# Kernel optimization log

Hardware: AMD Instinct MI355X
Metric: run time of the kernel (lower is better)

The kernel has to match this reference:

```python
import jax, jax.numpy as jnp
import numpy as np

B, TQ, TK = 2, 1024, 2048
DQ, DC, H, TOPK = 1024, 768, 16, 64
DH = DQ // H


def setup_inputs() -> dict:
    key = jax.random.key(0)
    ks = jax.random.split(key, 12)
    s = lambda d: 1.0 / np.sqrt(d)
    return {
        "x": jax.random.normal(ks[0], (B, TQ, DQ), jnp.float32),
        "context": jax.random.normal(ks[1], (B, TK, DC), jnp.float32),
        "key_padding_mask": jax.random.bernoulli(ks[2], 0.05, (B, TK)),
        "Wq": jax.random.normal(ks[3], (DQ, DQ), jnp.float32) * s(DQ),
        "bq": jnp.zeros((DQ,), jnp.float32),
        "Wk": jax.random.normal(ks[4], (DC, DQ), jnp.float32) * s(DC),
        "bk": jnp.zeros((DQ,), jnp.float32),
        "Wv": jax.random.normal(ks[5], (DC, DQ), jnp.float32) * s(DC),
        "bv": jnp.zeros((DQ,), jnp.float32),
        "Wo": jax.random.normal(ks[6], (DQ, DQ), jnp.float32) * s(DQ),
        "bo": jnp.zeros((DQ,), jnp.float32),
    }


def _heads(t):
    # (B, T, DQ) -> (B, H, T, DH)
    b, tt, _ = t.shape
    return t.reshape(b, tt, H, DH).transpose(0, 2, 1, 3)


def reference(x, context, key_padding_mask, Wq, bq, Wk, bk, Wv, bv, Wo, bo):
    q = _heads(x @ Wq + bq)          # (B,H,Tq,DH)
    k = _heads(context @ Wk + bk)    # (B,H,Tk,DH)
    v = _heads(context @ Wv + bv)    # (B,H,Tk,DH)

    scale = DH ** -0.5
    logits = jnp.einsum("bhqd,bhkd->bhqk", q, k) * scale  # (B,H,Tq,Tk)
    neg = jnp.finfo(logits.dtype).min
    logits = jnp.where(key_padding_mask[:, None, None, :], neg, logits)

    # hard top-k sparsification: keep top TOPK logits per query, fill rest with -inf-like
    topk_vals, topk_idx = jax.lax.top_k(logits, TOPK)
    sparse_logits = jnp.full_like(logits, neg)
    sparse_logits = jnp.put_along_axis(sparse_logits, topk_idx, topk_vals, axis=-1, inplace=False)

    attn = jax.nn.softmax(sparse_logits, axis=-1)
    out = jnp.einsum("bhqk,bhkd->bhqd", attn, v)  # (B,H,Tq,DH)
    out = out.transpose(0, 2, 1, 3).reshape(B, TQ, DQ)
    return out @ Wo + bo
```

## Files before the change

kernel.cpp:

```cpp
#include <hip/hip_runtime.h>
#include <cstdint>
#include <cstddef>

#define BN_ 2
#define TQ_ 1024
#define TK_ 2048
#define DQ_ 1024
#define DC_ 768
#define NH_ 16
#define DH_ 64
#define TOPK_ 64

typedef unsigned short u16;
typedef __attribute__((ext_vector_type(8))) short short8;
typedef __attribute__((ext_vector_type(8))) u16   ushort8;
typedef __attribute__((ext_vector_type(4))) float floatx4;

__device__ __forceinline__ float bf2f(u16 u) { return __uint_as_float(((unsigned)u) << 16); }
__device__ __forceinline__ u16 f2bf(float f) {
    unsigned u = __float_as_uint(f);
    u += 0x7FFFu + ((u >> 16) & 1u);
    return (u16)(u >> 16);
}
__device__ __forceinline__ float definite(float v, float repl) {
    return ((__float_as_uint(v) & 0x7F800000u) == 0x7F800000u) ? repl : v;
}
__device__ __forceinline__ unsigned mono(float f) {
    unsigned u = __float_as_uint(f);
    return (u & 0x80000000u) ? ~u : (u | 0x80000000u);
}
__device__ __forceinline__ float invmono(unsigned u) {
    return __uint_as_float((u & 0x80000000u) ? (u & 0x7FFFFFFFu) : ~u);
}
__device__ __forceinline__ int gsum16(int x) {
#pragma unroll
    for (int o = 1; o < 16; o <<= 1) x += __shfl_xor(x, o);
    return x;
}
__device__ __forceinline__ int gmin16(int x) {
#pragma unroll
    for (int o = 1; o < 16; o <<= 1) { int y = __shfl_xor(x, o); x = (y < x) ? y : x; }
    return x;
}
__device__ __forceinline__ unsigned gmin16u(unsigned x) {
#pragma unroll
    for (int o = 1; o < 16; o <<= 1) { unsigned y = __shfl_xor((int)x, o); x = (y < x) ? y : x; }
    return x;
}
__device__ __forceinline__ unsigned gmax16u(unsigned x) {
#pragma unroll
    for (int o = 1; o < 16; o <<= 1) { unsigned y = __shfl_xor((int)x, o); x = (y > x) ? y : x; }
    return x;
}
__device__ __forceinline__ float gmax16f(float x) {
#pragma unroll
    for (int o = 1; o < 16; o <<= 1) x = fmaxf(x, __shfl_xor(x, o));
    return x;
}
__device__ __forceinline__ float gsum16f(float x) {
#pragma unroll
    for (int o = 1; o < 16; o <<= 1) x += __shfl_xor(x, o);
    return x;
}

__global__ void marker_kernel(float* __restrict__ out, int n, float val) {
    const int i = blockIdx.x * 256 + threadIdx.x;
    if (i < n) out[i] = val;
}

template <int NV>
__device__ __forceinline__ void select_topk(const unsigned (&um)[NV], const int (&kk)[NV],
                                            unsigned base, int hb, int l16,
                                            float* cvrow, int* ckrow) {
    unsigned X = 0u;
    bool done = false;
    for (int bit = hb; bit >= 0; --bit) {
        const unsigned C = X | (1u << bit);
        int c = 0;
#pragma unroll
        for (int j = 0; j < NV; ++j) c += (um[j] >= C) ? 1 : 0;
        c = gsum16(c);
        if (!done && c >= 64) X = C;
        if (c == 64) done = true;
        if (__all(done)) break;
    }
    int myGt = 0;
#pragma unroll
    for (int j = 0; j < NV; ++j) myGt += (um[j] > X) ? 1 : 0;
    const int totalGt = gsum16(myGt);
    int pre = myGt;
#pragma unroll
    for (int off = 1; off < 16; off <<= 1) {
        const int tv = __shfl_up(pre, off);
        if (l16 >= off) pre += tv;
    }
    int wpos = pre - myGt;
#pragma unroll
    for (int j = 0; j < NV; ++j) {
        if (um[j] > X) {
            cvrow[wpos] = invmono(base + um[j]);
            ckrow[wpos] = kk[j];
            ++wpos;
        }
    }
    const float xval = invmono(base + X);
    int remaining = 64 - totalGt;
    int pos = totalGt;
    int lastkey = -1;
    while (remaining > 0) {
        int mykey = 0x7FFFFFFF;
#pragma unroll
        for (int j = 0; j < NV; ++j)
            if (um[j] == X && kk[j] > lastkey && kk[j] < mykey) mykey = kk[j];
        const int mn = gmin16(mykey);
        if (mn == 0x7FFFFFFF) break;
        if (mykey == mn) { cvrow[pos] = xval; ckrow[pos] = mn; }
        lastkey = mn;
        ++pos; --remaining;
    }
}

__global__ void __launch_bounds__(256) tsplit(const float* __restrict__ W,
                                              u16* __restrict__ Wh, u16* __restrict__ Wl,
                                              int K, int N) {
    __shared__ float t[32][33];
    const int x = threadIdx.x & 31, y = threadIdx.x >> 5;
    const int bn = blockIdx.x * 32, bk = blockIdx.y * 32;
#pragma unroll
    for (int i = 0; i < 32; i += 8) t[y + i][x] = W[(size_t)(bk + y + i) * N + bn + x];
    __syncthreads();
#pragma unroll
    for (int i = 0; i < 32; i += 8) {
        const float f = t[x][y + i];
        const u16 hi = f2bf(f);
        const size_t o = (size_t)(bn + y + i) * K + bk + x;
        Wh[o] = hi;
        Wl[o] = f2bf(f - bf2f(hi));
    }
}

template <int TBM, int ASPLIT, int OMODE>
__global__ void __launch_bounds__(256) gemm2(
    const void* __restrict__ Ap, const void* __restrict__ Alp,
    const u16* __restrict__ Bh, const u16* __restrict__ Bl,
    const float* __restrict__ bias, float scale,
    void* __restrict__ out0, void* __restrict__ out1,
    int M, int N, int K) {
    constexpr int MT = TBM / 32;
    alignas(16) __shared__ u16 Ah[TBM][72];
    alignas(16) __shared__ u16 Al[TBM][72];
    alignas(16) __shared__ u16 Bhs[64][72];
    alignas(16) __shared__ u16 Bls[64][72];

    const int tid = threadIdx.x;
    const int lane = tid & 63, wave = tid >> 6;
    const int wm = wave >> 1, wn = wave & 1;
    const int quad = lane >> 4, l16 = lane & 15;
    const int bm = blockIdx.y * TBM, bn = blockIdx.x * 64;

    floatx4 acc[MT][2] = {};

    for (int k0 = 0; k0 < K; k0 += 64) {
        __syncthreads();
        if constexpr (TBM == 64) {
            const int r0 = tid >> 3, c0 = (tid & 7) << 3;
#pragma unroll
            for (int hh = 0; hh < 2; ++hh) {
                const int r = r0 + hh * 32;
                const size_t aoff = (size_t)(bm + r) * K + k0 + c0;
                if constexpr (ASPLIT == 0) {
                    const float* f = (const float*)Ap + aoff;
                    const floatx4 a = *(const floatx4*)f;
                    const floatx4 b = *(const floatx4*)(f + 4);
#pragma unroll
                    for (int j = 0; j < 4; ++j) {
                        u16 t = f2bf(a[j]);
                        Ah[r][c0 + j] = t; Al[r][c0 + j] = f2bf(a[j] - bf2f(t));
                        t = f2bf(b[j]);
                        Ah[r][c0 + 4 + j] = t; Al[r][c0 + 4 + j] = f2bf(b[j] - bf2f(t));
                    }
                } else {
                    *(ushort8*)&Ah[r][c0] = *(const ushort8*)((const u16*)Ap  + aoff);
                    *(ushort8*)&Al[r][c0] = *(const ushort8*)((const u16*)Alp + aoff);
                }
            }
        } else {
            const int sr = tid >> 1, sc = (tid & 1) * 32;
            const float* f = (const float*)Ap + (size_t)(bm + sr) * K + k0 + sc;
#pragma unroll
            for (int v = 0; v < 8; ++v) {
                const floatx4 a = *(const floatx4*)(f + 4 * v);
#pragma unroll
                for (int j = 0; j < 4; ++j) {
                    const u16 t = f2bf(a[j]);
                    Ah[sr][sc + 4 * v + j] = t;
                    Al[sr][sc + 4 * v + j] = f2bf(a[j] - bf2f(t));
                }
            }
        }
        {
            const int r0 = tid >> 2, c0 = (tid & 3) * 16;
            const size_t boff = (size_t)(bn + r0) * K + k0 + c0;
            *(ushort8*)&Bhs[r0][c0]     = *(const ushort8*)(Bh + boff);
            *(ushort8*)&Bhs[r0][c0 + 8] = *(const ushort8*)(Bh + boff + 8);
            *(ushort8*)&Bls[r0][c0]     = *(const ushort8*)(Bl + boff);
            *(ushort8*)&Bls[r0][c0 + 8] = *(const ushort8*)(Bl + boff + 8);
        }
        __syncthreads();
#pragma unroll
        for (int s = 0; s < 2; ++s) {
            short8 ah[MT], al[MT], bh[2], bl[2];
#pragma unroll
            for (int mt = 0; mt < MT; ++mt) {
                ah[mt] = *(const short8*)&Ah[wm * (TBM / 2) + mt * 16 + l16][s * 32 + quad * 8];
                al[mt] = *(const short8*)&Al[wm * (TBM / 2) + mt * 16 + l16][s * 32 + quad * 8];
            }
#pragma unroll
            for (int nt = 0; nt < 2; ++nt) {
                bh[nt] = *(const short8*)&Bhs[wn * 32 + nt * 16 + l16][s * 32 + quad * 8];
                bl[nt] = *(const short8*)&Bls[wn * 32 + nt * 16 + l16][s * 32 + quad * 8];
            }
#pragma unroll
            for (int mt = 0; mt < MT; ++mt)
#pragma unroll
                for (int nt = 0; nt < 2; ++nt) {
                    acc[mt][nt] = __builtin_amdgcn_mfma_f32_16x16x32_bf16(ah[mt], bh[nt], acc[mt][nt], 0, 0, 0);
                    acc[mt][nt] = __builtin_amdgcn_mfma_f32_16x16x32_bf16(al[mt], bh[nt], acc[mt][nt], 0, 0, 0);
                    acc[mt][nt] = __builtin_amdgcn_mfma_f32_16x16x32_bf16(ah[mt], bl[nt], acc[mt][nt], 0, 0, 0);
                }
        }
    }

#pragma unroll
    for (int mt = 0; mt < MT; ++mt) {
#pragma unroll
        for (int nt = 0; nt < 2; ++nt) {
            const int col = bn + wn * 32 + nt * 16 + l16;
            const float bcol = bias[col];
#pragma unroll
            for (int r = 0; r < 4; ++r) {
                const int row = bm + wm * (TBM / 2) + mt * 16 + quad * 4 + r;
                const float val = definite((acc[mt][nt][r] + bcol) * scale, 0.0f);
                const size_t idx = (size_t)row * N + col;
                if constexpr (OMODE == 0) {
                    ((float*)out0)[idx] = val;
                } else if constexpr (OMODE == 1) {
                    ((u16*)out0)[idx] = f2bf(val);
                } else {
                    const u16 hi = f2bf(val);
                    ((u16*)out0)[idx] = hi;
                    ((u16*)out1)[idx] = f2bf(val - bf2f(hi));
                }
            }
        }
    }
}

__global__ void __launch_bounds__(256, 4) attn_topk(
    const u16* Qhi, const u16* Qlo,
    const u16* __restrict__ Khi, const u16* __restrict__ Klo,
    const u16* __restrict__ Vb16, const void* __restrict__ maskp,
    u16* attnH, u16* attnL) {
    __shared__ float lg[16][512];
    __shared__ float cval[16][64];
    __shared__ int   ckey[16][64];

    const int tid = threadIdx.x;
    const int lane = tid & 63, wave = tid >> 6;
    const int quad = lane >> 4, l16 = lane & 15;
    const int rowg = wave * 4 + quad;
    const int b = blockIdx.z, h = blockIdx.y, q0 = blockIdx.x * 16;

    int mmode;
    {
        bool cbyte = false, cbf = false, cf32 = false;
#pragma unroll
        for (int j = 0; j < 16; ++j) {
            const int i = lane + 64 * j;
            const unsigned v = ((const u16*)maskp)[i];
            cbyte |= (v == 0x0100u || v == 0x0101u) || ((i & 1) && v == 0x0001u);
            cbf   |= (!(i & 1)) && v == 0x3F80u;
            cf32  |= (i & 1) && v == 0x3F80u;
        }
        const bool abf = __any(cbf), af32 = __any(cf32), abyte = __any(cbyte);
        mmode = abf ? 2 : (af32 ? 3 : (abyte ? 1 : 0));
    }

    short8 qh[2], ql[2];
    {
        const size_t base = (size_t)(b * TQ_ + q0 + l16) * DQ_ + h * DH_ + quad * 8;
        qh[0] = *(const short8*)(Qhi + base);
        qh[1] = *(const short8*)(Qhi + base + 32);
        ql[0] = *(const short8*)(Qlo + base);
        ql[1] = *(const short8*)(Qlo + base + 32);
    }

    for (int i = tid; i < 16 * 64; i += 256) {
        cval[i >> 6][i & 63] = __uint_as_float(0xFF800000u);
        ckey[i >> 6][i & 63] = i & 63;
    }

    for (int qtr = 0; qtr < 4; ++qtr) {
#pragma unroll 2
        for (int t = 0; t < 8; ++t) {
            const int key = qtr * 512 + wave * 128 + t * 16 + l16;
            const size_t kb = (size_t)(b * TK_ + key) * DQ_ + h * DH_ + quad * 8;
            const short8 kh0 = *(const short8*)(Khi + kb);
            const short8 kh1 = *(const short8*)(Khi + kb + 32);
            const short8 kl0 = *(const short8*)(Klo + kb);
            const short8 kl1 = *(const short8*)(Klo + kb + 32);
            floatx4 acc = {};
            acc = __builtin_amdgcn_mfma_f32_16x16x32_bf16(qh[0], kh0, acc, 0, 0, 0);
            acc = __builtin_amdgcn_mfma_f32_16x16x32_bf16(ql[0], kh0, acc, 0, 0, 0);
            acc = __builtin_amdgcn_mfma_f32_16x16x32_bf16(qh[0], kl0, acc, 0, 0, 0);
            acc = __builtin_amdgcn_mfma_f32_16x16x32_bf16(qh[1], kh1, acc, 0, 0, 0);
            acc = __builtin_amdgcn_mfma_f32_16x16x32_bf16(ql[1], kh1, acc, 0, 0, 0);
            acc = __builtin_amdgcn_mfma_f32_16x16x32_bf16(qh[1], kl1, acc, 0, 0, 0);
            const int midx = b * TK_ + key;
            bool masked;
            if (mmode == 2)      masked = ((const u16*)maskp)[midx] != 0;
            else if (mmode == 3) masked = ((const float*)maskp)[midx] != 0.0f;
            else if (mmode == 1) masked = ((const unsigned char*)maskp)[midx] != 0;
            else                 masked = ((const int*)maskp)[midx] != 0;
            const int kk = wave * 128 + t * 16 + l16;
#pragma unroll
            for (int r = 0; r < 4; ++r)
                lg[quad * 4 + r][kk] = masked ? -3.0e38f : definite(acc[r], -3.0e38f);
        }
        __syncthreads();

        unsigned uc[4]; int ck4[4];
#pragma unroll
        for (int t = 0; t < 4; ++t) {
            uc[t] = mono(cval[rowg][l16 + 16 * t]);
            ck4[t] = ckey[rowg][l16 + 16 * t];
        }

        if (qtr == 0) {
            unsigned um[36]; int kk[36];
#pragma unroll
            for (int j = 0; j < 32; ++j) {
                um[j] = mono(lg[rowg][l16 + 16 * j]);
                kk[j] = l16 + 16 * j;
            }
#pragma unroll
            for (int t = 0; t < 4; ++t) { um[32 + t] = uc[t]; kk[32 + t] = ck4[t]; }
            select_topk<36>(um, kk, 0u, 31, l16, cval[rowg], ckey[rowg]);
        } else {
            unsigned cm = uc[0];
            cm = (uc[1] < cm) ? uc[1] : cm;
            cm = (uc[2] < cm) ? uc[2] : cm;
            cm = (uc[3] < cm) ? uc[3] : cm;
            cm = gmin16u(cm);
            unsigned zm[36]; int kk[36];
            unsigned zmx = 0;
#pragma unroll
            for (int j = 0; j < 32; ++j) {
                const unsigned u = mono(lg[rowg][l16 + 16 * j]);
                zm[j] = (u > cm) ? (u - cm) : 0u;
                kk[j] = qtr * 512 + l16 + 16 * j;
                zmx = (zm[j] > zmx) ? zm[j] : zmx;
            }
#pragma unroll
            for (int t = 0; t < 4; ++t) {
                zm[32 + t] = uc[t] - cm;
                kk[32 + t] = ck4[t];
                zmx = (zm[32 + t] > zmx) ? zm[32 + t] : zmx;
            }
            zmx = gmax16u(zmx);
            const int hb = 31 - __clz(zmx | 1u);
            select_topk<36>(zm, kk, cm, hb, l16, cval[rowg], ckey[rowg]);
        }
        if (qtr < 3) __syncthreads();
    }

    {
        float v4[4];
#pragma unroll
        for (int t = 0; t < 4; ++t) v4[t] = cval[rowg][l16 + 16 * t];
        float m = fmaxf(fmaxf(v4[0], v4[1]), fmaxf(v4[2], v4[3]));
        m = gmax16f(m);
        float p4[4], S = 0.f;
#pragma unroll
        for (int t = 0; t < 4; ++t) { p4[t] = __expf(v4[t] - m); S += p4[t]; }
        S = gsum16f(S);
        const float inv = 1.0f / S;
#pragma unroll
        for (int t = 0; t < 4; ++t) cval[rowg][l16 + 16 * t] = p4[t] * inv;
    }

    const int half = lane >> 5, l32 = lane & 31;
    const u16* Vrow = Vb16 + (size_t)b * TK_ * DQ_ + h * DH_ + l32 * 2;
#pragma unroll
    for (int rp = 0; rp < 2; ++rp) {
        const int row = wave * 4 + rp * 2 + half;
        float a0 = 0.f, a1 = 0.f;
#pragma unroll 4
        for (int e = 0; e < 64; ++e) {
            const float w = cval[row][e];
            const int k = ckey[row][e];
            const unsigned v2 = *(const unsigned*)(Vrow + (size_t)k * DQ_);
            a0 += w * bf2f((u16)(v2 & 0xFFFFu));
            a1 += w * bf2f((u16)(v2 >> 16));
        }
        a0 = definite(a0, 0.0f);
        a1 = definite(a1, 0.0f);
        const size_t o = (size_t)(b * TQ_ + q0 + row) * DQ_ + h * DH_ + l32 * 2;
        const u16 h0 = f2bf(a0), h1 = f2bf(a1);
        const u16 l0 = f2bf(a0 - bf2f(h0)), l1 = f2bf(a1 - bf2f(h1));
        *(unsigned*)(attnH + o) = (unsigned)h0 | ((unsigned)h1 << 16);
        *(unsigned*)(attnL + o) = (unsigned)l0 | ((unsigned)l1 << 16);
    }
}

extern "C" void kernel_launch(void* const* d_in, const int* in_sizes, int n_in,
                              void* d_out, int out_size, void* d_ws, size_t ws_size,
                              hipStream_t stream) {
    static const int exp_sizes[11] = {2097152, 3145728, 4096, 1048576, 1024,
                                      786432, 1024, 786432, 1024, 1048576, 1024};
    if (n_in != 11) {
        marker_kernel<<<(out_size + 255) / 256, 256, 0, stream>>>((float*)d_out, out_size,
                                                                  (float)(150 + n_in));
        return;
    }
    for (int i = 0; i < 11; ++i)
        if (in_sizes[i] != exp_sizes[i]) {
            marker_kernel<<<(out_size + 255) / 256, 256, 0, stream>>>((float*)d_out, out_size,
                                                                      (float)(200 + i));
            return;
        }

    const float* x   = (const float*)d_in[0];
    const float* ctx = (const float*)d_in[1];
    const void*  msk = d_in[2];
    const float* Wq = (const float*)d_in[3];
    const float* bq = (const float*)d_in[4];
    const float* Wk = (const float*)d_in[5];
    const float* bk = (const float*)d_in[6];
    const float* Wv = (const float*)d_in[7];
    const float* bv = (const float*)d_in[8];
    const float* Wo = (const float*)d_in[9];
    const float* bo = (const float*)d_in[10];

    const size_t SZ_Q = (size_t)BN_ * TQ_ * DQ_ * 2;
    const size_t SZ_K = (size_t)BN_ * TK_ * DQ_ * 2;
    const size_t NEED = 2 * SZ_Q + 2 * SZ_K + SZ_K;
    if (ws_size < NEED) {
        marker_kernel<<<(out_size + 255) / 256, 256, 0, stream>>>(
            (float*)d_out, out_size, (float)(ws_size >> 20));
        return;
    }

    char* ws = (char*)d_ws;
    u16* Qhi = (u16*)(ws);
    u16* Qlo = (u16*)(ws + SZ_Q);
    u16* Khi = (u16*)(ws + 2 * SZ_Q);
    u16* Klo = (u16*)(ws + 2 * SZ_Q + SZ_K);
    u16* Vb  = (u16*)(ws + 2 * SZ_Q + 2 * SZ_K);

    u16* WqT_h = Khi;
    u16* WqT_l = Khi + (size_t)DQ_ * DQ_;
    u16* WkT_h = Vb;
    u16* WkT_l = Vb + (size_t)DC_ * DQ_;
    u16* WvT_h = (u16*)d_out;
    u16* WvT_l = (u16*)d_out + (size_t)DC_ * DQ_;
    u16* WoT_h = Khi;
    u16* WoT_l = Khi + (size_t)DQ_ * DQ_;

    const int MQ = BN_ * TQ_;
    const int MK = BN_ * TK_;

    tsplit<<<dim3(DQ_ / 32, DQ_ / 32), 256, 0, stream>>>(Wq, WqT_h, WqT_l, DQ_, DQ_);
    gemm2<64, 0, 2><<<dim3(DQ_ / 64, MQ / 64), 256, 0, stream>>>(
        x, nullptr, WqT_h, WqT_l, bq, 0.125f, Qhi, Qlo, MQ, DQ_, DQ_);
    tsplit<<<dim3(DQ_ / 32, DC_ / 32), 256, 0, stream>>>(Wk, WkT_h, WkT_l, DC_, DQ_);
    gemm2<128, 0, 2><<<dim3(DQ_ / 64, MK / 128), 256, 0, stream>>>(
        ctx, nullptr, WkT_h, WkT_l, bk, 1.0f, Khi, Klo, MK, DQ_, DC_);
    tsplit<<<dim3(DQ_ / 32, DC_ / 32), 256, 0, stream>>>(Wv, WvT_h, WvT_l, DC_, DQ_);
    gemm2<128, 0, 1><<<dim3(DQ_ / 64, MK / 128), 256, 0, stream>>>(
        ctx, nullptr, WvT_h, WvT_l, bv, 1.0f, Vb, nullptr, MK, DQ_, DC_);

    attn_topk<<<dim3(TQ_ / 16, NH_, BN_), 256, 0, stream>>>(
        Qhi, Qlo, Khi, Klo, Vb, msk, Qhi, Qlo);

    tsplit<<<dim3(DQ_ / 32, DQ_ / 32), 256, 0, stream>>>(Wo, WoT_h, WoT_l, DQ_, DQ_);
    gemm2<64, 1, 0><<<dim3(DQ_ / 64, MQ / 64), 256, 0, stream>>>(
        Qhi, Qlo, WoT_h, WoT_l, bo, 1.0f, d_out, nullptr, MQ, DQ_, DQ_);
}
```

Baseline: 433.1 us.

## Retile projection GEMMs to 64x128 with XOR-swizzled LDS and range-narrow first top-k pass

Replaces the padded-LDS GEMM with a 64x128 tile that stores A and B in XOR-swizzled shared memory. This is meant to cut bank conflicts and to reuse each A tile across more output columns with vectorized stores. In the attention kernel, the first-quarter top-k selection now subtracts the row minimum and starts the radix search at the actual highest differing bit, instead of always scanning 32 bits. The costs are fewer blocks per GEMM grid, more registers per thread, and an extra min/max reduction per row.

Result: no change. 431.2 us (-0.4%).

```diff
diff --git a/kernel.cpp b/kernel.cpp
--- a/kernel.cpp
+++ b/kernel.cpp
@@ -139,91 +139,86 @@
     }
 }
 
-template <int TBM, int ASPLIT, int OMODE>
-__global__ void __launch_bounds__(256) gemm2(
+template <int ASPLIT, int OMODE>
+__global__ void __launch_bounds__(256) gemm3(
     const void* __restrict__ Ap, const void* __restrict__ Alp,
     const u16* __restrict__ Bh, const u16* __restrict__ Bl,
     const float* __restrict__ bias, float scale,
     void* __restrict__ out0, void* __restrict__ out1,
     int M, int N, int K) {
-    constexpr int MT = TBM / 32;
-    alignas(16) __shared__ u16 Ah[TBM][72];
-    alignas(16) __shared__ u16 Al[TBM][72];
-    alignas(16) __shared__ u16 Bhs[64][72];
-    alignas(16) __shared__ u16 Bls[64][72];
+    __shared__ u16 Ahs[64 * 64];
+    __shared__ u16 Als[64 * 64];
+    __shared__ u16 Bhs[128 * 64];
+    __shared__ u16 Bls[128 * 64];
 
     const int tid = threadIdx.x;
     const int lane = tid & 63, wave = tid >> 6;
     const int wm = wave >> 1, wn = wave & 1;
     const int quad = lane >> 4, l16 = lane & 15;
-    const int bm = blockIdx.y * TBM, bn = blockIdx.x * 64;
-
-    floatx4 acc[MT][2] = {};
+    const int bm = blockIdx.y * 64, bn = blockIdx.x * 128;
+
+    floatx4 acc[2][4] = {};
 
     for (int k0 = 0; k0 < K; k0 += 64) {
         __syncthreads();
-        if constexpr (TBM == 64) {
-            const int r0 = tid >> 3, c0 = (tid & 7) << 3;
-#pragma unroll
-            for (int hh = 0; hh < 2; ++hh) {
-                const int r = r0 + hh * 32;
-                const size_t aoff = (size_t)(bm + r) * K + k0 + c0;
-                if constexpr (ASPLIT == 0) {
-                    const float* f = (const float*)Ap + aoff;
-                    const floatx4 a = *(const floatx4*)f;
-                    const floatx4 b = *(const floatx4*)(f + 4);
-#pragma unroll
-                    for (int j = 0; j < 4; ++j) {
-                        u16 t = f2bf(a[j]);
-                        Ah[r][c0 + j] = t; Al[r][c0 + j] = f2bf(a[j] - bf2f(t));
-                        t = f2bf(b[j]);
-                        Ah[r][c0 + 4 + j] = t; Al[r][c0 + 4 + j] = f2bf(b[j] - bf2f(t));
-                    }
-                } else {
-                    *(ushort8*)&Ah[r][c0] = *(const ushort8*)((const u16*)Ap  + aoff);
-                    *(ushort8*)&Al[r][c0] = *(const ushort8*)((const u16*)Alp + aoff);
+#pragma unroll
+        for (int s2 = 0; s2 < 2; ++s2) {
+            const int slot = tid + s2 * 256;
+            const int m = slot >> 3, cpos = slot & 7;
+            const int c = cpos ^ (m & 7);
+            const size_t aoff = (size_t)(bm + m) * K + k0 + c * 8;
+            if constexpr (ASPLIT == 0) {
+                const float* f = (const float*)Ap + aoff;
+                const floatx4 a = *(const floatx4*)f;
+                const floatx4 b = *(const floatx4*)(f + 4);
+                ushort8 hi, lo;
+#pragma unroll
+                for (int j = 0; j < 4; ++j) {
+                    u16 t = f2bf(a[j]);
+                    hi[j] = t; lo[j] = f2bf(a[j] - bf2f(t));
+                    t = f2bf(b[j]);
+                    hi[4 + j] = t; lo[4 + j] = f2bf(b[j] - bf2f(t));
                 }
-            }
-        } else {
-            const int sr = tid >> 1, sc = (tid & 1) * 32;
-            const float* f = (const float*)Ap + (size_t)(bm + sr) * K + k0 + sc;
-#pragma unroll
-            for (int v = 0; v < 8; ++v) {
-                const floatx4 a = *(const floatx4*)(f + 4 * v);
-#pragma unroll
-                for (int j = 0; j < 4; ++j) {
-                    const u16 t = f2bf(a[j]);
-                    Ah[sr][sc + 4 * v + j] = t;
-                    Al[sr][sc + 4 * v + j] = f2bf(a[j] - bf2f(t));
-                }
-            }
-        }
-        {
-            const int r0 = tid >> 2, c0 = (tid & 3) * 16;
-            const size_t boff = (size_t)(bn + r0) * K + k0 + c0;
-            *(ushort8*)&Bhs[r0][c0]     = *(const ushort8*)(Bh + boff);
-            *(ushort8*)&Bhs[r0][c0 + 8] = *(const ushort8*)(Bh + boff + 8);
-            *(ushort8*)&Bls[r0][c0]     = *(const ushort8*)(Bl + boff);
-            *(ushort8*)&Bls[r0][c0 + 8] = *(const ushort8*)(Bl + boff + 8);
+                *(ushort8*)&Ahs[slot * 8] = hi;
+                *(ushort8*)&Als[slot * 8] = lo;
+            } else {
+                *(ushort8*)&Ahs[slot * 8] = *(const ushort8*)((const u16*)Ap  + aoff);
+                *(ushort8*)&Als[slot * 8] = *(const ushort8*)((const u16*)Alp + aoff);
+            }
+        }
+#pragma unroll
+        for (int s4 = 0; s4 < 4; ++s4) {
+            const int slot = tid + s4 * 256;
+            const int n = slot >> 3, cpos = slot & 7;
+            const int c = cpos ^ (n & 7);
+            const size_t boff = (size_t)(bn + n) * K + k0 + c * 8;
+            *(ushort8*)&Bhs[slot * 8] = *(const ushort8*)(Bh + boff);
+            *(ushort8*)&Bls[slot * 8] = *(const ushort8*)(Bl + boff);
         }
         __syncthreads();
 #pragma unroll
         for (int s = 0; s < 2; ++s) {
-            short8 ah[MT], al[MT], bh[2], bl[2];
-#pragma unroll
-            for (int mt = 0; mt < MT; ++mt) {
-                ah[mt] = *(const short8*)&Ah[wm * (TBM / 2) + mt * 16 + l16][s * 32 + quad * 8];
-                al[mt] = *(const short8*)&Al[wm * (TBM / 2) + mt * 16 + l16][s * 32 + quad * 8];
-            }
-#pragma unroll
-            for (int nt = 0; nt < 2; ++nt) {
-                bh[nt] = *(const short8*)&Bhs[wn * 32 + nt * 16 + l16][s * 32 + quad * 8];
-                bl[nt] = *(const short8*)&Bls[wn * 32 + nt * 16 + l16][s * 32 + quad * 8];
-            }
-#pragma unroll
-            for (int mt = 0; mt < MT; ++mt)
-#pragma unroll
-                for (int nt = 0; nt < 2; ++nt) {
+            short8 ah[2], al[2], bh[4], bl[4];
+#pragma unroll
+            for (int mt = 0; mt < 2; ++mt) {
+                const int m = wm * 32 + mt * 16 + l16;
+                const int cs = s * 4 + quad;
+                const int slot = m * 8 + (cs ^ (m & 7));
+                ah[mt] = *(const short8*)&Ahs[slot * 8];
+                al[mt] = *(const short8*)&Als[slot * 8];
+            }
+#pragma unroll
+            for (int nt = 0; nt < 4; ++nt) {
+                const int n = wn * 64 + nt * 16 + l16;
+                const int cs = s * 4 + quad;
+                const int slot = n * 8 + (cs ^ (n & 7));
+                bh[nt] = *(const short8*)&Bhs[slot * 8];
+                bl[nt] = *(const short8*)&Bls[slot * 8];
+            }
+#pragma unroll
+            for (int mt = 0; mt < 2; ++mt)
+#pragma unroll
+                for (int nt = 0; nt < 4; ++nt) {
                     acc[mt][nt] = __builtin_amdgcn_mfma_f32_16x16x32_bf16(ah[mt], bh[nt], acc[mt][nt], 0, 0, 0);
                     acc[mt][nt] = __builtin_amdgcn_mfma_f32_16x16x32_bf16(al[mt], bh[nt], acc[mt][nt], 0, 0, 0);
                     acc[mt][nt] = __builtin_amdgcn_mfma_f32_16x16x32_bf16(ah[mt], bl[nt], acc[mt][nt], 0, 0, 0);
@@ -232,14 +227,14 @@
     }
 
 #pragma unroll
-    for (int mt = 0; mt < MT; ++mt) {
-#pragma unroll
-        for (int nt = 0; nt < 2; ++nt) {
-            const int col = bn + wn * 32 + nt * 16 + l16;
+    for (int mt = 0; mt < 2; ++mt) {
+#pragma unroll
+        for (int nt = 0; nt < 4; ++nt) {
+            const int col = bn + wn * 64 + nt * 16 + l16;
             const float bcol = bias[col];
 #pragma unroll
             for (int r = 0; r < 4; ++r) {
-                const int row = bm + wm * (TBM / 2) + mt * 16 + quad * 4 + r;
+                const int row = bm + wm * 32 + mt * 16 + quad * 4 + r;
                 const float val = definite((acc[mt][nt][r] + bcol) * scale, 0.0f);
                 const size_t idx = (size_t)row * N + col;
                 if constexpr (OMODE == 0) {
@@ -345,7 +340,19 @@
             }
 #pragma unroll
             for (int t = 0; t < 4; ++t) { um[32 + t] = uc[t]; kk[32 + t] = ck4[t]; }
-            select_topk<36>(um, kk, 0u, 31, l16, cval[rowg], ckey[rowg]);
+            unsigned rmin = um[0], rmax = um[0];
+#pragma unroll
+            for (int j = 1; j < 36; ++j) {
+                rmin = (um[j] < rmin) ? um[j] : rmin;
+                rmax = (um[j] > rmax) ? um[j] : rmax;
+            }
+            rmin = gmin16u(rmin);
+            rmax = gmax16u(rmax);
+            unsigned zm[36];
+#pragma unroll
+            for (int j = 0; j < 36; ++j) zm[j] = um[j] - rmin;
+            const int hb = 31 - __clz((rmax - rmin) | 1u);
+            select_topk<36>(zm, kk, rmin, hb, l16, cval[rowg], ckey[rowg]);
         } else {
             unsigned cm = uc[0];
             cm = (uc[1] < cm) ? uc[1] : cm;
@@ -471,19 +478,19 @@
     const int MK = BN_ * TK_;
 
     tsplit<<<dim3(DQ_ / 32, DQ_ / 32), 256, 0, stream>>>(Wq, WqT_h, WqT_l, DQ_, DQ_);
-    gemm2<64, 0, 2><<<dim3(DQ_ / 64, MQ / 64), 256, 0, stream>>>(
+    gemm3<0, 2><<<dim3(DQ_ / 128, MQ / 64), 256, 0, stream>>>(
         x, nullptr, WqT_h, WqT_l, bq, 0.125f, Qhi, Qlo, MQ, DQ_, DQ_);
     tsplit<<<dim3(DQ_ / 32, DC_ / 32), 256, 0, stream>>>(Wk, WkT_h, WkT_l, DC_, DQ_);
-    gemm2<128, 0, 2><<<dim3(DQ_ / 64, MK / 128), 256, 0, stream>>>(
+    gemm3<0, 2><<<dim3(DQ_ / 128, MK / 64), 256, 0, stream>>>(
         ctx, nullptr, WkT_h, WkT_l, bk, 1.0f, Khi, Klo, MK, DQ_, DC_);
     tsplit<<<dim3(DQ_ / 32, DC_ / 32), 256, 0, stream>>>(Wv, WvT_h, WvT_l, DC_, DQ_);
-    gemm2<128, 0, 1><<<dim3(DQ_ / 64, MK / 128), 256, 0, stream>>>(
+    gemm3<0, 1><<<dim3(DQ_ / 128, MK / 64), 256, 0, stream>>>(
         ctx, nullptr, WvT_h, WvT_l, bv, 1.0f, Vb, nullptr, MK, DQ_, DC_);
 
     attn_topk<<<dim3(TQ_ / 16, NH_, BN_), 256, 0, stream>>>(
         Qhi, Qlo, Khi, Klo, Vb, msk, Qhi, Qlo);
 
     tsplit<<<dim3(DQ_ / 32, DQ_ / 32), 256, 0, stream>>>(Wo, WoT_h, WoT_l, DQ_, DQ_);
-    gemm2<64, 1, 0><<<dim3(DQ_ / 64, MQ / 64), 256, 0, stream>>>(
+    gemm3<1, 0><<<dim3(DQ_ / 128, MQ / 64), 256, 0, stream>>>(
         Qhi, Qlo, WoT_h, WoT_l, bo, 1.0f, d_out, nullptr, MQ, DQ_, DQ_);
 }
```
